# Performance work log

Hardware: AMD Instinct MI355X
Metric: run time of the kernel (lower is better)

The kernel has to match this reference:

```python
import jax, jax.numpy as jnp
from jax import lax
import numpy as np

B, T, I, H = 512, 512, 128, 256


def setup_inputs() -> dict:
    key = jax.random.key(0)
    ks = jax.random.split(key, 7)
    s = 1.0 / np.sqrt(H)  # pytorch-style init scale
    return {
        "x": jax.random.normal(ks[0], (B, T, I), dtype=jnp.float32),
        "h0": jax.random.normal(ks[1], (1, B, H), dtype=jnp.float32),
        "c0": jax.random.normal(ks[2], (1, B, H), dtype=jnp.float32),
        "w_ih": jax.random.normal(ks[3], (4 * H, I), dtype=jnp.float32) * s,
        "w_hh": jax.random.normal(ks[4], (4 * H, H), dtype=jnp.float32) * s,
        "b_ih": jax.random.normal(ks[5], (4 * H,), dtype=jnp.float32) * s,
        "b_hh": jax.random.normal(ks[6], (4 * H,), dtype=jnp.float32) * s,
    }


def reference(x, h0, c0, w_ih, w_hh, b_ih, b_hh):
    """Single-layer LSTM; returns final cell state c_n of shape [1, B, H].
    Gate row order in w_*/b_* is PyTorch's (i, f, g, o) blocks of H."""
    h = h0[0]  # [B, H]
    c = c0[0]  # [B, H]
    # Precompute input contribution for all timesteps: [T, B, 4H]
    xg = jnp.einsum('bti,gi->tbg', x, w_ih) + (b_ih + b_hh)

    def step(carry, xg_t):
        h, c = carry
        g = xg_t + h @ w_hh.T  # [B, 4H]
        gi, gf, gg, go = jnp.split(g, 4, axis=-1)
        c_new = jax.nn.sigmoid(gf) * c + jax.nn.sigmoid(gi) * jnp.tanh(gg)
        h_new = jax.nn.sigmoid(go) * jnp.tanh(c_new)
        return (h_new, c_new), None

    (h_T, c_T), _ = lax.scan(step, (h, c), xg)
    return c_T[None]  # [1, B, H]
```

## Files before the change

kernel.cpp:

```cpp
#include <hip/hip_runtime.h>
#include <hip/hip_bf16.h>
#include <hip/hip_fp16.h>


typedef __attribute__((ext_vector_type(4))) float f32x4;
typedef __attribute__((ext_vector_type(8))) _Float16 f16x8;
typedef __attribute__((ext_vector_type(4))) unsigned int u32x4;
typedef __attribute__((ext_vector_type(4))) int i32x4;

static __device__ __forceinline__ float h2f(unsigned short u) {
  return (float)__builtin_bit_cast(_Float16, u);
}
static __device__ __forceinline__ unsigned short f2h(float f) {
  return __builtin_bit_cast(unsigned short, (_Float16)f);
}
static __device__ __forceinline__ float fast_sigmoid(float x) {
  return __builtin_amdgcn_rcpf(1.0f + __builtin_amdgcn_exp2f(-1.44269504f * x));
}
static __device__ __forceinline__ float fast_tanh(float x) {
  return 1.0f - 2.0f * __builtin_amdgcn_rcpf(1.0f + __builtin_amdgcn_exp2f(2.88539008f * x));
}

__global__ __launch_bounds__(256) void prep1(
    const float* __restrict__ whh, const float* __restrict__ h0,
    const float* __restrict__ wih, const float* __restrict__ bih,
    const float* __restrict__ bhh,
    float* __restrict__ scl, unsigned short* __restrict__ wih_h,
    float* __restrict__ bcv) {
  const int b = blockIdx.x, tid = threadIdx.x;
  if (b < 192) {
    __shared__ float s[256];
    const float* src = (b < 128) ? whh : h0;
    int base = (b < 128) ? b * 2048 : (b - 128) * 2048;
    float m = 0.f;
#pragma unroll
    for (int i = 0; i < 8; ++i) m = fmaxf(m, fabsf(src[base + i * 256 + tid]));
    s[tid] = m; __syncthreads();
    for (int w = 128; w > 0; w >>= 1) {
      if (tid < w) s[tid] = fmaxf(s[tid], s[tid + w]);
      __syncthreads();
    }
    if (tid == 0) scl[8 + b] = s[0];
  } else {
    int i = ((b - 192) * 256 + tid) * 4;
    int q = i >> 7, k = i & 127;
    int p = (q & 3) * 256 + (q >> 2);
    f32x4 v = *(const f32x4*)(wih + p * 128 + k);
    ushort4 pk;
    pk.x = f2h(v[0]); pk.y = f2h(v[1]); pk.z = f2h(v[2]); pk.w = f2h(v[3]);
    *(ushort4*)(wih_h + i) = pk;
    if (b == 192) {
      for (int q2 = tid; q2 < 1024; q2 += 256) {
        int p2 = (q2 & 3) * 256 + (q2 >> 2);
        bcv[q2] = bih[p2] + bhh[p2];
      }
    }
  }
}

__global__ __launch_bounds__(256) void prep2(
    const float* __restrict__ whh, const float* __restrict__ h0,
    const float* __restrict__ c0, float* __restrict__ scl,
    signed char* __restrict__ wq, signed char* __restrict__ hst,
    float* __restrict__ cst) {
  __shared__ float s[256];
  const int b = blockIdx.x, tid = threadIdx.x;
  float v = (tid < 128) ? scl[8 + tid] : 0.f;
  s[tid] = v; __syncthreads();
  for (int w = 128; w > 0; w >>= 1) {
    if (tid < w) s[tid] = fmaxf(s[tid], s[tid + w]);
    __syncthreads();
  }
  float sw = s[0]; __syncthreads();
  v = (tid < 64) ? scl[136 + tid] : 0.f;
  s[tid] = v; __syncthreads();
  for (int w = 128; w > 0; w >>= 1) {
    if (tid < w) s[tid] = fmaxf(s[tid], s[tid + w]);
    __syncthreads();
  }
  float sh = s[0];
  if (b == 0 && tid == 0) { scl[0] = sw; scl[1] = sh; }

  const float invw = 127.0f / sw;
  int base = b * 1024;
#pragma unroll
  for (int i = 0; i < 4; ++i) {
    int idx = base + i * 256 + tid;
    int q = (int)rintf(whh[idx] * invw);
    wq[idx] = (signed char)max(-127, min(127, q));
  }
  const float invh = 127.0f / sh;
  int sb = b * 512;
#pragma unroll
  for (int i = 0; i < 2; ++i) {
    int idx = sb + i * 256 + tid;
    int q = (int)rintf(h0[idx] * invh);
    hst[idx] = (signed char)max(-127, min(127, q));
    cst[idx] = c0[idx];
  }
}

__global__ __launch_bounds__(256) void xgemm(
    const float* __restrict__ x, const unsigned short* __restrict__ wih,
    const float* __restrict__ bconv,
    unsigned short* __restrict__ xg, int t0, int tclog) {
  __shared__ unsigned short Ash[128 * 128];
  __shared__ unsigned short Bsh[128 * 128];

  const int tid  = threadIdx.x;
  const int lane = tid & 63;
  const int wv   = tid >> 6;
  const int c16  = lane & 15;
  const int gq   = lane >> 4;
  const long m0  = (long)blockIdx.x * 128;
  const int tcm  = (1 << tclog) - 1;

#pragma unroll
  for (int i = 0; i < 16; ++i) {
    int fidx = (i * 256 + tid) * 4;
    int row = fidx >> 7, k = fidx & 127;
    long cr = m0 + row;
    long b  = cr >> tclog;
    long tl = cr & tcm;
    f32x4 v = *(const f32x4*)(x + ((size_t)b * 512 + t0 + tl) * 128 + k);
    ushort4 pk;
    pk.x = f2h(v[0]); pk.y = f2h(v[1]); pk.z = f2h(v[2]); pk.w = f2h(v[3]);
    int byte = (row * 256 + k * 2) ^ ((row & 7) << 4);
    *(ushort4*)((char*)Ash + byte) = pk;
  }

  const int mh = (wv >> 1) * 64;
  const int nh = (wv & 1) * 64;

  for (int nc = 0; nc < 8; ++nc) {
    __syncthreads();
    {
      const char* wb = (const char*)(wih + nc * 128 * 128);
#pragma unroll
      for (int i = 0; i < 8; ++i) {
        int idx16 = i * 256 + tid;
        int row = idx16 >> 4, ch = idx16 & 15;
        int srcoff = row * 256 + ((ch * 16) ^ ((row & 7) << 4));
        u32x4 v = *(const u32x4*)(wb + srcoff);
        *(u32x4*)((char*)Bsh + idx16 * 16) = v;
      }
    }
    __syncthreads();

    float bias_v[4];
#pragma unroll
    for (int nt = 0; nt < 4; ++nt)
      bias_v[nt] = bconv[nc * 128 + nh + nt * 16 + c16];

    f16x8 af[4][4], bfr[4][4];
#pragma unroll
    for (int sm = 0; sm < 4; ++sm)
#pragma unroll
      for (int kt = 0; kt < 4; ++kt) {
        int m = mh + sm * 16 + c16;
        int byte = (m * 256 + (kt * 32 + gq * 8) * 2) ^ ((m & 7) << 4);
        af[sm][kt] = __builtin_bit_cast(f16x8, *(const u32x4*)((const char*)Ash + byte));
      }
#pragma unroll
    for (int nt = 0; nt < 4; ++nt)
#pragma unroll
      for (int kt = 0; kt < 4; ++kt) {
        int n = nh + nt * 16 + c16;
        int byte = (n * 256 + (kt * 32 + gq * 8) * 2) ^ ((n & 7) << 4);
        bfr[nt][kt] = __builtin_bit_cast(f16x8, *(const u32x4*)((const char*)Bsh + byte));
      }

    f32x4 acc[4][4];
#pragma unroll
    for (int sm = 0; sm < 4; ++sm)
#pragma unroll
      for (int nt = 0; nt < 4; ++nt) { f32x4 z = {0.f, 0.f, 0.f, 0.f}; acc[sm][nt] = z; }
#pragma unroll
    for (int sm = 0; sm < 4; ++sm)
#pragma unroll
      for (int nt = 0; nt < 4; ++nt)
#pragma unroll
        for (int kt = 0; kt < 4; ++kt)
          acc[sm][nt] = __builtin_amdgcn_mfma_f32_16x16x32_f16(af[sm][kt], bfr[nt][kt], acc[sm][nt], 0, 0, 0);

#pragma unroll
    for (int sm = 0; sm < 4; ++sm)
#pragma unroll
      for (int nt = 0; nt < 4; ++nt) {
        long row = m0 + mh + sm * 16 + gq * 4;
        int gcol = nc * 128 + nh + nt * 16 + c16;
#pragma unroll
        for (int r = 0; r < 4; ++r)
          xg[(size_t)(row + r) * 1024 + gcol] = f2h(acc[sm][nt][r] + bias_v[nt]);
      }
  }
}

__global__ __launch_bounds__(512)
__attribute__((amdgpu_waves_per_eu(2, 2)))
void fused_chunk(
    const unsigned short* __restrict__ xgc, const signed char* __restrict__ wq,
    const float* __restrict__ scales, signed char* __restrict__ hst,
    float* __restrict__ cst, float* __restrict__ out, int Tc, int first, int last,
    const float* __restrict__ x, const unsigned short* __restrict__ wih,
    const float* __restrict__ bconv, unsigned short* __restrict__ xgn,
    int t0n, int tclog, int do_x) {
  __shared__ char smem[65536];

  const int tid  = threadIdx.x;
  const int lane = tid & 63;
  const int wv   = tid >> 6;
  const int c16  = lane & 15;
  const int gq   = lane >> 4;

  if (blockIdx.x < 128) {
    signed char (*hb)[1280] = (signed char (*)[1280])smem;
    const int b0 = blockIdx.x * 4;

    const int col = wv * 32 + c16;
    float cv0 = cst[(b0 + gq) * 256 + col];
    float cv1 = cst[(b0 + gq) * 256 + col + 16];

    const float sw   = scales[0] * (1.0f / 127.0f);
    const float facR = sw * (1.0f / 127.0f);
    const float fac0 = first ? sw * (scales[1] * (1.0f / 127.0f)) : facR;

    i32x4 wf[8][4];
#pragma unroll
    for (int nt = 0; nt < 8; ++nt)
#pragma unroll
      for (int kt = 0; kt < 4; ++kt) {
        int n = (nt >> 1) * 256 + wv * 32 + (nt & 1) * 16 + c16;
        wf[nt][kt] = *(const i32x4*)(wq + n * 256 + kt * 64 + gq * 16);
      }
#pragma unroll
    for (int nt = 0; nt < 8; ++nt)
#pragma unroll
      for (int kt = 0; kt < 4; ++kt)
        asm volatile("" : "+v"(wf[nt][kt]));
    asm volatile("" ::: "memory");

    for (int i = tid; i < 1024; i += 512) {
      int row = i >> 8, cc = i & 255;
      hb[0][row * 320 + cc] = hst[(b0 + row) * 256 + cc];
    }

    const char* pxp = (const char*)(xgc + ((size_t)(b0 + gq) * Tc) * 1024 + col * 4);
    ushort4 px0 = *(const ushort4*)pxp;
    ushort4 px1 = *(const ushort4*)(pxp + 128);
    pxp += 2048;

    const bool mrow = (c16 & 3) == 0;
    const int  hrow = c16 >> 2;
    i32x4 af[4];
#pragma unroll
    for (int kt = 0; kt < 4; ++kt) { i32x4 z = {0, 0, 0, 0}; af[kt] = z; }
    const i32x4 zacc = {0, 0, 0, 0};
    int q0 = 0, q1 = 0;

    __syncthreads();

    for (int tt = 0; tt < Tc; ++tt) {
      const int cur = tt & 1;

      if (mrow) {
        const signed char* hp = &hb[cur][hrow * 320 + gq * 16];
        af[0] = *(const i32x4*)(hp);
        af[1] = *(const i32x4*)(hp + 64);
        af[2] = *(const i32x4*)(hp + 128);
        af[3] = *(const i32x4*)(hp + 192);
      }

      ushort4 pn0 = *(const ushort4*)pxp;
      ushort4 pn1 = *(const ushort4*)(pxp + 128);
      pxp += 2048;

      i32x4 acc[8];
#pragma unroll
      for (int ne = 0; ne < 4; ++ne)
        acc[2 * ne] = __builtin_amdgcn_mfma_i32_16x16x64_i8(af[0], wf[2 * ne][0], zacc, 0, 0, 0);
#pragma unroll
      for (int kt = 1; kt < 4; ++kt)
#pragma unroll
        for (int ne = 0; ne < 4; ++ne)
          acc[2 * ne] = __builtin_amdgcn_mfma_i32_16x16x64_i8(af[kt], wf[2 * ne][kt], acc[2 * ne], 0, 0, 0);
#pragma unroll
      for (int ne = 0; ne < 4; ++ne)
        acc[2 * ne + 1] = __builtin_amdgcn_mfma_i32_16x16x64_i8(af[0], wf[2 * ne + 1][0], zacc, 0, 0, 0);
#pragma unroll
      for (int kt = 1; kt < 4; ++kt)
#pragma unroll
        for (int ne = 0; ne < 4; ++ne)
          acc[2 * ne + 1] = __builtin_amdgcn_mfma_i32_16x16x64_i8(af[kt], wf[2 * ne + 1][kt], acc[2 * ne + 1], 0, 0, 0);

      const float fac = (tt == 0) ? fac0 : facR;

      {
        float gi = __builtin_fmaf((float)acc[0][0], fac, h2f(px0.x));
        float gf = __builtin_fmaf((float)acc[2][0], fac, h2f(px0.y));
        float gg = __builtin_fmaf((float)acc[4][0], fac, h2f(px0.z));
        float go = __builtin_fmaf((float)acc[6][0], fac, h2f(px0.w));
        cv0 = fast_sigmoid(gf) * cv0 + fast_sigmoid(gi) * fast_tanh(gg);
        float hn = fast_sigmoid(go) * fast_tanh(cv0);
        q0 = (int)rintf(hn * 127.0f);
        hb[cur ^ 1][gq * 320 + col] = (signed char)q0;
      }
      {
        float gi = __builtin_fmaf((float)acc[1][0], fac, h2f(px1.x));
        float gf = __builtin_fmaf((float)acc[3][0], fac, h2f(px1.y));
        float gg = __builtin_fmaf((float)acc[5][0], fac, h2f(px1.z));
        float go = __builtin_fmaf((float)acc[7][0], fac, h2f(px1.w));
        cv1 = fast_sigmoid(gf) * cv1 + fast_sigmoid(gi) * fast_tanh(gg);
        float hn = fast_sigmoid(go) * fast_tanh(cv1);
        q1 = (int)rintf(hn * 127.0f);
        hb[cur ^ 1][gq * 320 + col + 16] = (signed char)q1;
      }

      px0 = pn0; px1 = pn1;
      __syncthreads();
    }

    cst[(b0 + gq) * 256 + col]      = cv0;
    cst[(b0 + gq) * 256 + col + 16] = cv1;
    hst[(b0 + gq) * 256 + col]      = (signed char)q0;
    hst[(b0 + gq) * 256 + col + 16] = (signed char)q1;
    if (last) {
      out[(b0 + gq) * 256 + col]      = cv0;
      out[(b0 + gq) * 256 + col + 16] = cv1;
    }
  } else if (do_x) {
    unsigned short* Ash = (unsigned short*)smem;
    unsigned short* Bsh = (unsigned short*)(smem + 32768);
    const int tcm    = (1 << tclog) - 1;
    const int ntiles = Tc << 2;
    const int wm = wv >> 2, wn = wv & 3;
    const int mh = wm * 64, nh = wn * 32;

    for (int rt = (int)blockIdx.x - 128; rt < ntiles; rt += 128) {
      const long m0 = (long)rt * 128;
      __syncthreads();

#pragma unroll
      for (int i = 0; i < 8; ++i) {
        int fidx = (i * 512 + tid) * 4;
        int row = fidx >> 7, k = fidx & 127;
        long cr = m0 + row;
        long b  = cr >> tclog;
        long tl = cr & tcm;
        f32x4 v = *(const f32x4*)(x + ((size_t)b * 512 + t0n + tl) * 128 + k);
        ushort4 pk;
        pk.x = f2h(v[0]); pk.y = f2h(v[1]); pk.z = f2h(v[2]); pk.w = f2h(v[3]);
        int byte = (row * 256 + k * 2) ^ ((row & 7) << 4);
        *(ushort4*)((char*)Ash + byte) = pk;
      }

      for (int nc = 0; nc < 8; ++nc) {
        __syncthreads();
        {
          const char* wb = (const char*)(wih + nc * 128 * 128);
#pragma unroll
          for (int i = 0; i < 4; ++i) {
            int idx16 = i * 512 + tid;
            int row = idx16 >> 4, ch = idx16 & 15;
            int srcoff = row * 256 + ((ch * 16) ^ ((row & 7) << 4));
            u32x4 v = *(const u32x4*)(wb + srcoff);
            *(u32x4*)((char*)Bsh + idx16 * 16) = v;
          }
        }
        __syncthreads();

        float bias_v[2];
#pragma unroll
        for (int nt = 0; nt < 2; ++nt)
          bias_v[nt] = bconv[nc * 128 + nh + nt * 16 + c16];

        f16x8 af[4][4], bfr[2][4];
#pragma unroll
        for (int sm = 0; sm < 4; ++sm)
#pragma unroll
          for (int kt = 0; kt < 4; ++kt) {
            int m = mh + sm * 16 + c16;
            int byte = (m * 256 + (kt * 32 + gq * 8) * 2) ^ ((m & 7) << 4);
            af[sm][kt] = __builtin_bit_cast(f16x8, *(const u32x4*)((const char*)Ash + byte));
          }
#pragma unroll
        for (int nt = 0; nt < 2; ++nt)
#pragma unroll
          for (int kt = 0; kt < 4; ++kt) {
            int n = nh + nt * 16 + c16;
            int byte = (n * 256 + (kt * 32 + gq * 8) * 2) ^ ((n & 7) << 4);
            bfr[nt][kt] = __builtin_bit_cast(f16x8, *(const u32x4*)((const char*)Bsh + byte));
          }

        f32x4 acc[4][2];
#pragma unroll
        for (int sm = 0; sm < 4; ++sm)
#pragma unroll
          for (int nt = 0; nt < 2; ++nt) { f32x4 z = {0.f, 0.f, 0.f, 0.f}; acc[sm][nt] = z; }
#pragma unroll
        for (int sm = 0; sm < 4; ++sm)
#pragma unroll
          for (int nt = 0; nt < 2; ++nt)
#pragma unroll
            for (int kt = 0; kt < 4; ++kt)
              acc[sm][nt] = __builtin_amdgcn_mfma_f32_16x16x32_f16(af[sm][kt], bfr[nt][kt], acc[sm][nt], 0, 0, 0);

#pragma unroll
        for (int sm = 0; sm < 4; ++sm)
#pragma unroll
          for (int nt = 0; nt < 2; ++nt) {
            long row = m0 + mh + sm * 16 + gq * 4;
            int gcol = nc * 128 + nh + nt * 16 + c16;
#pragma unroll
            for (int r = 0; r < 4; ++r)
              xgn[(size_t)(row + r) * 1024 + gcol] = f2h(acc[sm][nt][r] + bias_v[nt]);
          }
      }
    }
  }
}

extern "C" void kernel_launch(void* const* d_in, const int* in_sizes, int n_in,
                              void* d_out, int out_size, void* d_ws, size_t ws_size,
                              hipStream_t stream) {
  const float* x   = (const float*)d_in[0];
  const float* h0  = (const float*)d_in[1];
  const float* c0  = (const float*)d_in[2];
  const float* wih = (const float*)d_in[3];
  const float* whh = (const float*)d_in[4];
  const float* bih = (const float*)d_in[5];
  const float* bhh = (const float*)d_in[6];
  float* out = (float*)d_out;

  const size_t fixed = 262144u  + 262144u  + 131072u
                     + 524288u  + 4096u  + 1024u ;
  int tc = 128;
  while (tc > 4 && 2u * (size_t)512 * tc * 2048 + fixed > ws_size) tc >>= 1;
  int tclog = 31 - __builtin_clz((unsigned)tc);
  size_t bufsz = (size_t)512 * tc * 2048;

  char* ws = (char*)d_ws;
  unsigned short* xgb0  = (unsigned short*)ws;
  unsigned short* xgb1  = (unsigned short*)(ws + bufsz);
  size_t off = 2u * bufsz;
  unsigned short* wih_h = (unsigned short*)(ws + off);  off += 262144u;
  signed char*    wqb   = (signed char*)(ws + off);     off += 262144u;
  signed char*    hst   = (signed char*)(ws + off);     off += 131072u;
  float*          cst   = (float*)(ws + off);           off += 524288u;
  float*          bcv   = (float*)(ws + off);           off += 4096u;
  float*          scl   = (float*)(ws + off);

  prep1<<<320, 256, 0, stream>>>(whh, h0, wih, bih, bhh, scl, wih_h, bcv);
  prep2<<<256, 256, 0, stream>>>(whh, h0, c0, scl, wqb, hst, cst);

  xgemm<<<4 * tc, 256, 0, stream>>>(x, wih_h, bcv, xgb0, 0, tclog);

  int NC = 512 / tc;
  for (int c = 0; c < NC; ++c) {
    unsigned short* cur = (c & 1) ? xgb1 : xgb0;
    unsigned short* nxt = (c & 1) ? xgb0 : xgb1;
    int do_x = (c + 1 < NC) ? 1 : 0;
    fused_chunk<<<256, 512, 0, stream>>>(
        cur, wqb, scl, hst, cst, out, tc, (c == 0) ? 1 : 0, (c == NC - 1) ? 1 : 0,
        x, wih_h, bcv, nxt, (c + 1) * tc, tclog, do_x);
  }
}
```

Baseline: 531.3 us.

## Permute W_hh rows so each lane owns adjacent columns; vectorize h/c/xg accesses

The prep kernel now permutes recurrent weight rows so each lane's two MFMA output tiles map to adjacent hidden columns (2*c16, 2*c16+1) instead of columns 16 apart. The recurrent loop then loads its xg gate values with one 16-byte load, writes both quantized h bytes to LDS as one 16-bit store, and reads and writes c with float2. The LDS row pitch shrinks from 320 to 288, and the waves_per_eu(2,2) attribute is dropped. The aim is fewer memory and LDS instructions on the serial per-timestep path, at the cost of possible LDS bank-conflict changes and different register allocation.

```diff
diff --git a/kernel.cpp b/kernel.cpp
--- a/kernel.cpp
+++ b/kernel.cpp
@@ -86,7 +86,11 @@
 #pragma unroll
   for (int i = 0; i < 4; ++i) {
     int idx = base + i * 256 + tid;
-    int q = (int)rintf(whh[idx] * invw);
+    int nr = idx >> 8, k = idx & 255;
+    int g = nr >> 8, r = nr & 255;
+    int wvv = r >> 5, ntc = (r >> 4) & 1, cc = r & 15;
+    int src = g * 256 + wvv * 32 + 2 * cc + ntc;
+    int q = (int)rintf(whh[src * 256 + k] * invw);
     wq[idx] = (signed char)max(-127, min(127, q));
   }
   const float invh = 127.0f / sh;
@@ -197,7 +201,6 @@
 }
 
 __global__ __launch_bounds__(512)
-__attribute__((amdgpu_waves_per_eu(2, 2)))
 void fused_chunk(
     const unsigned short* __restrict__ xgc, const signed char* __restrict__ wq,
     const float* __restrict__ scales, signed char* __restrict__ hst,
@@ -214,12 +217,11 @@
   const int gq   = lane >> 4;
 
   if (blockIdx.x < 128) {
-    signed char (*hb)[1280] = (signed char (*)[1280])smem;
+    signed char (*hb)[1152] = (signed char (*)[1152])smem;
     const int b0 = blockIdx.x * 4;
 
-    const int col = wv * 32 + c16;
-    float cv0 = cst[(b0 + gq) * 256 + col];
-    float cv1 = cst[(b0 + gq) * 256 + col + 16];
+    const int colA = wv * 32 + 2 * c16;
+    float2 cv = *(const float2*)&cst[(b0 + gq) * 256 + colA];
 
     const float sw   = scales[0] * (1.0f / 127.0f);
     const float facR = sw * (1.0f / 127.0f);
@@ -242,12 +244,12 @@
 
     for (int i = tid; i < 1024; i += 512) {
       int row = i >> 8, cc = i & 255;
-      hb[0][row * 320 + cc] = hst[(b0 + row) * 256 + cc];
-    }
-
-    const char* pxp = (const char*)(xgc + ((size_t)(b0 + gq) * Tc) * 1024 + col * 4);
-    ushort4 px0 = *(const ushort4*)pxp;
-    ushort4 px1 = *(const ushort4*)(pxp + 128);
+      hb[0][row * 288 + cc] = hst[(b0 + row) * 256 + cc];
+    }
+
+    const char* pxp = (const char*)xgc +
+        (((size_t)(b0 + gq) * Tc) * 1024 + (size_t)colA * 4) * 2;
+    u32x4 px = *(const u32x4*)pxp;
     pxp += 2048;
 
     const bool mrow = (c16 & 3) == 0;
@@ -256,7 +258,7 @@
 #pragma unroll
     for (int kt = 0; kt < 4; ++kt) { i32x4 z = {0, 0, 0, 0}; af[kt] = z; }
     const i32x4 zacc = {0, 0, 0, 0};
-    int q0 = 0, q1 = 0;
+    unsigned short hpack = 0;
 
     __syncthreads();
 
@@ -264,15 +266,14 @@
       const int cur = tt & 1;
 
       if (mrow) {
-        const signed char* hp = &hb[cur][hrow * 320 + gq * 16];
+        const signed char* hp = &hb[cur][hrow * 288 + gq * 16];
         af[0] = *(const i32x4*)(hp);
         af[1] = *(const i32x4*)(hp + 64);
         af[2] = *(const i32x4*)(hp + 128);
         af[3] = *(const i32x4*)(hp + 192);
       }
 
-      ushort4 pn0 = *(const ushort4*)pxp;
-      ushort4 pn1 = *(const ushort4*)(pxp + 128);
+      u32x4 pn = *(const u32x4*)pxp;
       pxp += 2048;
 
       i32x4 acc[8];
@@ -295,38 +296,36 @@
 
       const float fac = (tt == 0) ? fac0 : facR;
 
+      int q0, q1;
       {
-        float gi = __builtin_fmaf((float)acc[0][0], fac, h2f(px0.x));
-        float gf = __builtin_fmaf((float)acc[2][0], fac, h2f(px0.y));
-        float gg = __builtin_fmaf((float)acc[4][0], fac, h2f(px0.z));
-        float go = __builtin_fmaf((float)acc[6][0], fac, h2f(px0.w));
-        cv0 = fast_sigmoid(gf) * cv0 + fast_sigmoid(gi) * fast_tanh(gg);
-        float hn = fast_sigmoid(go) * fast_tanh(cv0);
+        float gi = __builtin_fmaf((float)acc[0][0], fac, h2f((unsigned short)(px[0] & 0xffff)));
+        float gf = __builtin_fmaf((float)acc[2][0], fac, h2f((unsigned short)(px[0] >> 16)));
+        float gg = __builtin_fmaf((float)acc[4][0], fac, h2f((unsigned short)(px[1] & 0xffff)));
+        float go = __builtin_fmaf((float)acc[6][0], fac, h2f((unsigned short)(px[1] >> 16)));
+        cv.x = fast_sigmoid(gf) * cv.x + fast_sigmoid(gi) * fast_tanh(gg);
+        float hn = fast_sigmoid(go) * fast_tanh(cv.x);
         q0 = (int)rintf(hn * 127.0f);
-        hb[cur ^ 1][gq * 320 + col] = (signed char)q0;
       }
       {
-        float gi = __builtin_fmaf((float)acc[1][0], fac, h2f(px1.x));
-        float gf = __builtin_fmaf((float)acc[3][0], fac, h2f(px1.y));
-        float gg = __builtin_fmaf((float)acc[5][0], fac, h2f(px1.z));
-        float go = __builtin_fmaf((float)acc[7][0], fac, h2f(px1.w));
-        cv1 = fast_sigmoid(gf) * cv1 + fast_sigmoid(gi) * fast_tanh(gg);
-        float hn = fast_sigmoid(go) * fast_tanh(cv1);
+        float gi = __builtin_fmaf((float)acc[1][0], fac, h2f((unsigned short)(px[2] & 0xffff)));
+        float gf = __builtin_fmaf((float)acc[3][0], fac, h2f((unsigned short)(px[2] >> 16)));
+        float gg = __builtin_fmaf((float)acc[5][0], fac, h2f((unsigned short)(px[3] & 0xffff)));
+        float go = __builtin_fmaf((float)acc[7][0], fac, h2f((unsigned short)(px[3] >> 16)));
+        cv.y = fast_sigmoid(gf) * cv.y + fast_sigmoid(gi) * fast_tanh(gg);
+        float hn = fast_sigmoid(go) * fast_tanh(cv.y);
         q1 = (int)rintf(hn * 127.0f);
-        hb[cur ^ 1][gq * 320 + col + 16] = (signed char)q1;
-      }
-
-      px0 = pn0; px1 = pn1;
+      }
+      hpack = (unsigned short)((q0 & 0xff) | ((q1 & 0xff) << 8));
+      *(unsigned short*)&hb[cur ^ 1][gq * 288 + colA] = hpack;
+
+      px = pn;
       __syncthreads();
     }
 
-    cst[(b0 + gq) * 256 + col]      = cv0;
-    cst[(b0 + gq) * 256 + col + 16] = cv1;
-    hst[(b0 + gq) * 256 + col]      = (signed char)q0;
-    hst[(b0 + gq) * 256 + col + 16] = (signed char)q1;
+    *(float2*)&cst[(b0 + gq) * 256 + colA] = cv;
+    *(unsigned short*)&hst[(b0 + gq) * 256 + colA] = hpack;
     if (last) {
-      out[(b0 + gq) * 256 + col]      = cv0;
-      out[(b0 + gq) * 256 + col + 16] = cv1;
+      *(float2*)&out[(b0 + gq) * 256 + colA] = cv;
     }
   } else if (do_x) {
     unsigned short* Ash = (unsigned short*)smem;
```

After: 526.2 us. No clear change (-1.0%).
